# Optimization experiments

Measured on AMD Instinct MI355X. Metric: run time of the kernel, lower is better.

Reference implementation:

```python
import jax, jax.numpy as jnp
import numpy as np

INC, OUTC, NHEADS, KSIZE = 256, 256, 8, 5


def setup_inputs() -> dict:
    key = jax.random.key(0)
    k1, k2 = jax.random.split(key, 2)
    x = jax.random.normal(k1, (4, INC, 64, 64), dtype=jnp.float32)
    w_qkv = jax.random.normal(k2, (3 * OUTC, INC), dtype=jnp.float32) * 0.02
    b_qkv = jnp.zeros((3 * OUTC,), dtype=jnp.float32)
    return {"x": x, "w_qkv": w_qkv, "b_qkv": b_qkv}


def reference(x, w_qkv, b_qkv):
    N, Cin, H, W = x.shape
    hd = OUTC // NHEADS
    ofs = KSIZE // 2
    K2 = KSIZE * KSIZE

    # 1x1 conv == pointwise matmul over channels
    qkv = jnp.einsum('nchw,dc->ndhw', x, w_qkv) + b_qkv[None, :, None, None]
    Q = qkv[:, :OUTC]
    K = qkv[:, OUTC:2 * OUTC]
    V = qkv[:, 2 * OUTC:]

    # Zero-pad K/V; track validity so boundary softmax only spans in-bounds
    # positions (the torch code slices smaller windows at borders -> no pad
    # contribution to softmax).
    Kp = jnp.pad(K, ((0, 0), (0, 0), (ofs, ofs), (ofs, ofs)))
    Vp = jnp.pad(V, ((0, 0), (0, 0), (ofs, ofs), (ofs, ofs)))
    valid = jnp.pad(jnp.ones((H, W), dtype=bool), ((ofs, ofs), (ofs, ofs)))

    # Sliding windows via KSIZE^2 static shifted slices: [N,D,H,W,K2]
    k_win = jnp.stack([Kp[:, :, dy:dy + H, dx:dx + W]
                       for dy in range(KSIZE) for dx in range(KSIZE)], axis=-1)
    v_win = jnp.stack([Vp[:, :, dy:dy + H, dx:dx + W]
                       for dy in range(KSIZE) for dx in range(KSIZE)], axis=-1)
    m_win = jnp.stack([valid[dy:dy + H, dx:dx + W]
                       for dy in range(KSIZE) for dx in range(KSIZE)], axis=-1)  # [H,W,K2]

    qh = Q.reshape(N, NHEADS, hd, H, W)
    kh = k_win.reshape(N, NHEADS, hd, H, W, K2)
    vh = v_win.reshape(N, NHEADS, hd, H, W, K2)

    scores = jnp.einsum('ngdhw,ngdhwk->nghwk', qh, kh)          # [N,G,H,W,K2]
    scores = jnp.where(m_win[None, None], scores, -jnp.inf)
    att = jax.nn.softmax(scores, axis=-1)
    out = jnp.einsum('nghwk,ngdhwk->ngdhw', att, vh)            # [N,G,hd,H,W]
    return out.reshape(N, OUTC, H, W)
```

## Files before the change

### kernel.cpp

```cpp
#include <hip/hip_runtime.h>
#include <hip/hip_bf16.h>
#include <math.h>

#define CIN 256
#define COUT 768
#define OUTC 256
#define HH 64
#define WW 64
#define HW 4096

typedef unsigned int uint32;
typedef unsigned short ushort16;
typedef unsigned long long u64;

using short8 = __attribute__((ext_vector_type(8))) short;
using f32x4  = __attribute__((ext_vector_type(4))) float;
using hf2    = __attribute__((ext_vector_type(2))) _Float16;

__device__ inline uint32 pkbf2(float a, float b) {
    __hip_bfloat162 h = __float22bfloat162_rn(make_float2(a, b));
    union { __hip_bfloat162 h2; uint32 u; } cv; cv.h2 = h;
    return cv.u;
}
__device__ inline uint32 pkhf2(float a, float b) {
    union { _Float16 h[2]; uint32 u; } cv;
    cv.h[0] = (_Float16)a; cv.h[1] = (_Float16)b;
    return cv.u;
}
__device__ inline float dpp_xor1(float x) {
#if __has_builtin(__builtin_amdgcn_update_dpp)
    int i = __builtin_amdgcn_update_dpp(0, __float_as_int(x),
                                        0xB1, 0xF, 0xF, true);
    return __int_as_float(i);
#else
    return __shfl_xor(x, 1, 64);
#endif
}
__device__ inline float dot2acc(hf2 a, hf2 b, float c) {
#if __has_builtin(__builtin_amdgcn_fdot2)
    return __builtin_amdgcn_fdot2(a, b, c, false);
#else
    c = fmaf((float)a[0], (float)b[0], c);
    return fmaf((float)a[1], (float)b[1], c);
#endif
}

#define LDSTR 40

__global__ __launch_bounds__(256) void qkv_gemm_kernel(
    const float* __restrict__ x, const float* __restrict__ wq,
    const float* __restrict__ bq, ushort16* __restrict__ qkv)
{
    __shared__ __align__(16) char smem[32768];
    ushort16* As = (ushort16*)smem;
    ushort16* Bs = (ushort16*)smem + 128 * LDSTR;

    const int n   = blockIdx.z;
    const int d0  = blockIdx.y * 128;
    const int p0  = blockIdx.x * 128;
    const int tid = threadIdx.x;
    const int lane = tid & 63;
    const int wid  = tid >> 6;
    const int wm = wid >> 1;
    const int wn = wid & 1;

    const float* xb = x + (size_t)n * CIN * HW;

    const int arow = tid >> 2;
    const int akk  = (tid & 3) * 8;
    const float* aptr = wq + (size_t)(d0 + arow) * CIN + akk;
    const int bkg = (tid >> 6) * 8;
    const int bpg = (tid & 63) * 2;
    const float* bptr = xb + (size_t)bkg * HW + p0 + bpg;

    ushort16* awr0 = &As[arow * LDSTR + akk];
    ushort16* awr1 = &As[(arow + 64) * LDSTR + akk];
    ushort16* bwr0 = &Bs[bpg * LDSTR + bkg];
    ushort16* bwr1 = &Bs[(bpg + 1) * LDSTR + bkg];

    f32x4 acc[4][4];
    #pragma unroll
    for (int i = 0; i < 4; ++i)
        #pragma unroll
        for (int j = 0; j < 4; ++j) acc[i][j] = (f32x4){0.f, 0.f, 0.f, 0.f};

    const int lrow = lane & 15;
    const int lk   = (lane >> 4) * 8;

    float4 a0[4], a1[4];
    float2 b0[8], b1[8];

#define LOAD_SET(aS, bS, ko) do {                                         \
        aS[0] = *(const float4*)(aptr + (ko));                            \
        aS[1] = *(const float4*)(aptr + (ko) + 4);                        \
        aS[2] = *(const float4*)(aptr + (size_t)64 * CIN + (ko));         \
        aS[3] = *(const float4*)(aptr + (size_t)64 * CIN + (ko) + 4);     \
        _Pragma("unroll")                                                 \
        for (int j = 0; j < 8; ++j)                                       \
            bS[j] = *(const float2*)(bptr + (size_t)((ko) + j) * HW);     \
    } while (0)

#define WRITE_SET(aS, bS) do {                                            \
        uint32 w0 = pkbf2(aS[0].x, aS[0].y), w1 = pkbf2(aS[0].z, aS[0].w);\
        uint32 w2 = pkbf2(aS[1].x, aS[1].y), w3 = pkbf2(aS[1].z, aS[1].w);\
        *(uint4*)awr0 = make_uint4(w0, w1, w2, w3);                       \
        w0 = pkbf2(aS[2].x, aS[2].y); w1 = pkbf2(aS[2].z, aS[2].w);       \
        w2 = pkbf2(aS[3].x, aS[3].y); w3 = pkbf2(aS[3].z, aS[3].w);       \
        *(uint4*)awr1 = make_uint4(w0, w1, w2, w3);                       \
        uint4 c0, c1;                                                     \
        c0.x = pkbf2(bS[0].x, bS[1].x); c0.y = pkbf2(bS[2].x, bS[3].x);   \
        c0.z = pkbf2(bS[4].x, bS[5].x); c0.w = pkbf2(bS[6].x, bS[7].x);   \
        c1.x = pkbf2(bS[0].y, bS[1].y); c1.y = pkbf2(bS[2].y, bS[3].y);   \
        c1.z = pkbf2(bS[4].y, bS[5].y); c1.w = pkbf2(bS[6].y, bS[7].y);   \
        *(uint4*)bwr0 = c0;                                               \
        *(uint4*)bwr1 = c1;                                               \
    } while (0)

#define COMPUTE() do {                                                    \
        short8 af[4], bf[4];                                              \
        _Pragma("unroll")                                                 \
        for (int fm = 0; fm < 4; ++fm)                                    \
            af[fm] = *(const short8*)&As[(wm * 64 + fm * 16 + lrow) * LDSTR + lk]; \
        _Pragma("unroll")                                                 \
        for (int fn = 0; fn < 4; ++fn)                                    \
            bf[fn] = *(const short8*)&Bs[(wn * 64 + fn * 16 + lrow) * LDSTR + lk]; \
        _Pragma("unroll")                                                 \
        for (int fm = 0; fm < 4; ++fm)                                    \
            _Pragma("unroll")                                             \
            for (int fn = 0; fn < 4; ++fn)                                \
                acc[fm][fn] = __builtin_amdgcn_mfma_f32_16x16x32_bf16(    \
                    af[fm], bf[fn], acc[fm][fn], 0, 0, 0);                \
    } while (0)

    LOAD_SET(a0, b0, 0);
    LOAD_SET(a1, b1, 32);

    #pragma unroll 1
    for (int kt = 0; kt < 8; kt += 2) {
        __syncthreads();
        WRITE_SET(a0, b0);
        if (kt + 2 < 8) LOAD_SET(a0, b0, (kt + 2) * 32);
        __syncthreads();
        COMPUTE();

        __syncthreads();
        WRITE_SET(a1, b1);
        if (kt + 3 < 8) LOAD_SET(a1, b1, (kt + 3) * 32);
        __syncthreads();
        COMPUTE();
    }
#undef LOAD_SET
#undef WRITE_SET
#undef COMPUTE

    __syncthreads();

    u64* E = (u64*)smem + (size_t)wid * 1024;

    const int hi4 = lane >> 4;
    #pragma unroll
    for (int fm = 0; fm < 4; ++fm) {
        const int D = d0 + wm * 64 + fm * 16 + hi4 * 4;
        const float4 bias = *(const float4*)(&bq[D]);
        const int cell = fm * 2 + (hi4 >> 1);
        const int half = hi4 & 1;
        #pragma unroll
        for (int fn = 0; fn < 4; ++fn) {
            const int pl = fn * 16 + lrow;
            f32x4 v = acc[fm][fn];
            u64 pk = (u64)pkhf2(v[0] + bias.x, v[1] + bias.y)
                   | ((u64)pkhf2(v[2] + bias.z, v[3] + bias.w) << 32);
            E[pl * 16 + (cell ^ (pl & 7)) * 2 + half] = pk;
        }
    }
    const int pl4 = lane >> 2;
    const int dq  = lane & 3;
    ushort16* qn = qkv + (size_t)n * COUT * HW;
    #pragma unroll
    for (int s = 0; s < 2; ++s) {
        const int D = d0 + wm * 64 + s * 32;
        const int slot = D >> 5;
        ushort16* sb2 = qn + (size_t)slot * (HW * 32);
        #pragma unroll
        for (int g = 0; g < 4; ++g) {
            const int prow = g * 16 + pl4;
            const int c = s * 4 + dq;
            const uint4 val = *(const uint4*)&E[prow * 16 + ((c ^ (prow & 7)) * 2)];
            *(uint4*)(sb2 + (size_t)(p0 + wn * 64 + prow) * 32 + dq * 8) = val;
        }
    }
}

#define TR 4
#define TC 32
#define HR 8
#define HC 36
#define NPIX (HR*HC)

__global__ __launch_bounds__(256) void attn_kernel(
    const ushort16* __restrict__ qkv, float* __restrict__ out)
{
    __shared__ uint4 Ks[NPIX * 4];
    __shared__ uint4 Vs[NPIX * 4];

    const int n    = blockIdx.z;
    const int head = blockIdx.y;
    const int ht = blockIdx.x >> 1;
    const int wt = blockIdx.x & 1;
    const int h0 = ht * TR;
    const int w0 = wt * TC;

    const int tid  = threadIdx.x;
    const int half = tid & 1;
    const int wc   = (tid >> 1) & 31;
    const int tr   = tid >> 6;

    const int h = h0 + tr, w = w0 + wc;
    const int p = h * WW + w;

    const uint4* Kb = (const uint4*)(qkv + ((size_t)(n * 24 + 8 + head)) * HW * 32);
    const uint4* Vb = (const uint4*)(qkv + ((size_t)(n * 24 + 16 + head)) * HW * 32);

    for (int c = tid; c < 2 * NPIX * 4; c += 256) {
        const int b  = (c >= NPIX * 4);
        const int cc = c - b * NPIX * 4;
        const int pix = cc >> 2, i = cc & 3;
        const int hr = pix / HC, cw = pix - hr * HC;
        const int hh = h0 + hr - 2, ww = w0 + cw - 2;
        if (hh >= 0 && hh < HH && ww >= 0 && ww < WW) {
            const int pp = hh * WW + ww;
            const uint4 v = (b ? Vb : Kb)[(size_t)pp * 4 + i];
            const int unit = (pix * 4 + i) ^ (pix & 7);
            (b ? Vs : Ks)[unit] = v;
        }
    }

    hf2 q[8];
    {
        const uint4* Qp = (const uint4*)(qkv + (((size_t)(n * 24 + head)) * HW + p) * 32);
        union { uint4 u; hf2 h[4]; } c0, c1;
        c0.u = Qp[half * 2];
        c1.u = Qp[half * 2 + 1];
        #pragma unroll
        for (int i = 0; i < 4; ++i) { q[i] = c0.h[i]; q[4 + i] = c1.h[i]; }
    }

    __syncthreads();

    float sc[25];
    #pragma unroll
    for (int ky = 0; ky < 5; ++ky) {
        const int hh = h + ky - 2;
        const int hr = tr + ky;
        #pragma unroll
        for (int kx = 0; kx < 5; ++kx) {
            const int ww = w + kx - 2;
            float s;
            if (hh >= 0 && hh < HH && ww >= 0 && ww < WW) {
                const int pix = hr * HC + (wc + kx);
                const int u0 = (pix * 4 + half * 2)     ^ (pix & 7);
                const int u1 = (pix * 4 + half * 2 + 1) ^ (pix & 7);
                union { uint4 u; hf2 h[4]; } a, b;
                a.u = Ks[u0]; b.u = Ks[u1];
                float t = 0.f;
                t = dot2acc(q[0], a.h[0], t);
                t = dot2acc(q[1], a.h[1], t);
                t = dot2acc(q[2], a.h[2], t);
                t = dot2acc(q[3], a.h[3], t);
                t = dot2acc(q[4], b.h[0], t);
                t = dot2acc(q[5], b.h[1], t);
                t = dot2acc(q[6], b.h[2], t);
                t = dot2acc(q[7], b.h[3], t);
                s = t;
            } else {
                s = -1e30f;
            }
            sc[ky * 5 + kx] = s;
        }
    }
    #pragma unroll
    for (int k = 0; k < 25; ++k) {
        float o = dpp_xor1(sc[k]);
        sc[k] = (sc[k] <= -1e29f) ? sc[k] : sc[k] + o;
    }

    float m = sc[0];
    #pragma unroll
    for (int k = 1; k < 25; ++k) m = fmaxf(m, sc[k]);
    float sum = 0.f;
    #pragma unroll
    for (int k = 0; k < 25; ++k) {
        float e = __expf(sc[k] - m);
        sc[k] = e;
        sum += e;
    }
    const float inv = 1.f / sum;

    hf2 acch[8];
    #pragma unroll
    for (int i = 0; i < 8; ++i) acch[i] = (hf2){(_Float16)0.f, (_Float16)0.f};
    #pragma unroll
    for (int ky = 0; ky < 5; ++ky) {
        const int hh = h + ky - 2;
        if (hh < 0 || hh >= HH) continue;
        const int hr = tr + ky;
        #pragma unroll
        for (int kx = 0; kx < 5; ++kx) {
            const int ww = w + kx - 2;
            if (ww < 0 || ww >= WW) continue;
            const _Float16 af = (_Float16)sc[ky * 5 + kx];
            const hf2 ah = (hf2){af, af};
            const int pix = hr * HC + (wc + kx);
            const int u0 = (pix * 4 + half * 2)     ^ (pix & 7);
            const int u1 = (pix * 4 + half * 2 + 1) ^ (pix & 7);
            union { uint4 u; hf2 h[4]; } xv, yv;
            xv.u = Vs[u0]; yv.u = Vs[u1];
            acch[0] += ah * xv.h[0];
            acch[1] += ah * xv.h[1];
            acch[2] += ah * xv.h[2];
            acch[3] += ah * xv.h[3];
            acch[4] += ah * yv.h[0];
            acch[5] += ah * yv.h[1];
            acch[6] += ah * yv.h[2];
            acch[7] += ah * yv.h[3];
        }
    }

    float* Ob = out + ((size_t)(n * 8 + head) * 32 + half * 16) * HW + p;
    #pragma unroll
    for (int i = 0; i < 8; ++i) {
        Ob[(size_t)(2*i)   * HW] = (float)acch[i][0] * inv;
        Ob[(size_t)(2*i+1) * HW] = (float)acch[i][1] * inv;
    }
}

extern "C" void kernel_launch(void* const* d_in, const int* in_sizes, int n_in,
                              void* d_out, int out_size, void* d_ws, size_t ws_size,
                              hipStream_t stream) {
    const float* x  = (const float*)d_in[0];
    const float* wq = (const float*)d_in[1];
    const float* bq = (const float*)d_in[2];
    float* out = (float*)d_out;
    ushort16* qkv = (ushort16*)d_ws;

    dim3 g1(HW / 128, COUT / 128, 4);
    qkv_gemm_kernel<<<g1, 256, 0, stream>>>(x, wq, bq, qkv);

    dim3 g2(32, 8, 4);
    attn_kernel<<<g2, 256, 0, stream>>>(qkv, out);
}
```

Baseline: 41.49 us.

## Split head dim over four lanes, halve attention tile, share one LDS buffer for K then V

The attention kernel now assigns four threads per pixel, each holding 8 of the 32 head channels, and reduces the partial scores with two DPP xor steps. Tiles shrink to 4x16 pixels, so the grid doubles to 2048 blocks. A single shared buffer first holds K, then is refilled with V that was prefetched into registers during the score phase, which cuts LDS per block. Score and AV loops run at raised wave priority. In exchange the halo overhead per pixel grows (20 columns loaded for 16 output) and two extra barriers are added.

```diff
diff --git a/kernel.cpp b/kernel.cpp
--- a/kernel.cpp
+++ b/kernel.cpp
@@ -34,6 +34,15 @@
     return __int_as_float(i);
 #else
     return __shfl_xor(x, 1, 64);
+#endif
+}
+__device__ inline float dpp_xor2(float x) {
+#if __has_builtin(__builtin_amdgcn_update_dpp)
+    int i = __builtin_amdgcn_update_dpp(0, __float_as_int(x),
+                                        0x4E, 0xF, 0xF, true);
+    return __int_as_float(i);
+#else
+    return __shfl_xor(x, 2, 64);
 #endif
 }
 __device__ inline float dot2acc(hf2 a, hf2 b, float c) {
@@ -192,61 +201,72 @@
 }
 
 #define TR 4
-#define TC 32
+#define TC 16
 #define HR 8
-#define HC 36
+#define HC 20
 #define NPIX (HR*HC)
+#define NCELL (NPIX*4)
 
 __global__ __launch_bounds__(256) void attn_kernel(
     const ushort16* __restrict__ qkv, float* __restrict__ out)
 {
-    __shared__ uint4 Ks[NPIX * 4];
-    __shared__ uint4 Vs[NPIX * 4];
+    __shared__ uint4 KVs[NCELL];
 
     const int n    = blockIdx.z;
     const int head = blockIdx.y;
-    const int ht = blockIdx.x >> 1;
-    const int wt = blockIdx.x & 1;
+    const int ht = blockIdx.x >> 2;
+    const int wt = blockIdx.x & 3;
     const int h0 = ht * TR;
     const int w0 = wt * TC;
 
     const int tid  = threadIdx.x;
-    const int half = tid & 1;
-    const int wc   = (tid >> 1) & 31;
-    const int tr   = tid >> 6;
-
+    const int quar = tid & 3;
+    const int pid  = tid >> 2;
+    const int tr = pid >> 4, wc = pid & 15;
     const int h = h0 + tr, w = w0 + wc;
     const int p = h * WW + w;
 
+    const uint4* Qb = (const uint4*)(qkv + ((size_t)(n * 24 + head)) * HW * 32);
     const uint4* Kb = (const uint4*)(qkv + ((size_t)(n * 24 + 8 + head)) * HW * 32);
     const uint4* Vb = (const uint4*)(qkv + ((size_t)(n * 24 + 16 + head)) * HW * 32);
 
-    for (int c = tid; c < 2 * NPIX * 4; c += 256) {
-        const int b  = (c >= NPIX * 4);
-        const int cc = c - b * NPIX * 4;
-        const int pix = cc >> 2, i = cc & 3;
-        const int hr = pix / HC, cw = pix - hr * HC;
-        const int hh = h0 + hr - 2, ww = w0 + cw - 2;
-        if (hh >= 0 && hh < HH && ww >= 0 && ww < WW) {
-            const int pp = hh * WW + ww;
-            const uint4 v = (b ? Vb : Kb)[(size_t)pp * 4 + i];
-            const int unit = (pix * 4 + i) ^ (pix & 7);
-            (b ? Vs : Ks)[unit] = v;
-        }
-    }
-
-    hf2 q[8];
+    #pragma unroll
+    for (int it = 0; it < 3; ++it) {
+        const int c = tid + it * 256;
+        if (c < NCELL) {
+            const int pix = c >> 2, i = c & 3;
+            const int hr = pix / HC, cw = pix - hr * HC;
+            const int hh = h0 + hr - 2, ww = w0 + cw - 2;
+            if (hh >= 0 && hh < HH && ww >= 0 && ww < WW) {
+                const int pp = hh * WW + ww;
+                KVs[(pix * 4 + i) ^ (pix & 7)] = Kb[(size_t)pp * 4 + i];
+            }
+        }
+    }
+    uint4 vreg[3];
+    #pragma unroll
+    for (int it = 0; it < 3; ++it) {
+        const int c = tid + it * 256;
+        if (c < NCELL) {
+            const int pix = c >> 2, i = c & 3;
+            const int hr = pix / HC, cw = pix - hr * HC;
+            const int hh = h0 + hr - 2, ww = w0 + cw - 2;
+            if (hh >= 0 && hh < HH && ww >= 0 && ww < WW)
+                vreg[it] = Vb[(size_t)(hh * WW + ww) * 4 + i];
+        }
+    }
+
+    hf2 q[4];
     {
-        const uint4* Qp = (const uint4*)(qkv + (((size_t)(n * 24 + head)) * HW + p) * 32);
-        union { uint4 u; hf2 h[4]; } c0, c1;
-        c0.u = Qp[half * 2];
-        c1.u = Qp[half * 2 + 1];
-        #pragma unroll
-        for (int i = 0; i < 4; ++i) { q[i] = c0.h[i]; q[4 + i] = c1.h[i]; }
+        union { uint4 u; hf2 h[4]; } c;
+        c.u = Qb[(size_t)p * 4 + quar];
+        #pragma unroll
+        for (int i = 0; i < 4; ++i) q[i] = c.h[i];
     }
 
     __syncthreads();
 
+    __builtin_amdgcn_s_setprio(1);
     float sc[25];
     #pragma unroll
     for (int ky = 0; ky < 5; ++ky) {
@@ -255,33 +275,36 @@
         #pragma unroll
         for (int kx = 0; kx < 5; ++kx) {
             const int ww = w + kx - 2;
-            float s;
-            if (hh >= 0 && hh < HH && ww >= 0 && ww < WW) {
+            const bool valid = (hh >= 0 && hh < HH && ww >= 0 && ww < WW);
+            float t = 0.f;
+            if (valid) {
                 const int pix = hr * HC + (wc + kx);
-                const int u0 = (pix * 4 + half * 2)     ^ (pix & 7);
-                const int u1 = (pix * 4 + half * 2 + 1) ^ (pix & 7);
-                union { uint4 u; hf2 h[4]; } a, b;
-                a.u = Ks[u0]; b.u = Ks[u1];
-                float t = 0.f;
-                t = dot2acc(q[0], a.h[0], t);
-                t = dot2acc(q[1], a.h[1], t);
-                t = dot2acc(q[2], a.h[2], t);
-                t = dot2acc(q[3], a.h[3], t);
-                t = dot2acc(q[4], b.h[0], t);
-                t = dot2acc(q[5], b.h[1], t);
-                t = dot2acc(q[6], b.h[2], t);
-                t = dot2acc(q[7], b.h[3], t);
-                s = t;
-            } else {
-                s = -1e30f;
+                union { uint4 u; hf2 hh2[4]; } a;
+                a.u = KVs[(pix * 4 + quar) ^ (pix & 7)];
+                t = dot2acc(q[0], a.hh2[0], t);
+                t = dot2acc(q[1], a.hh2[1], t);
+                t = dot2acc(q[2], a.hh2[2], t);
+                t = dot2acc(q[3], a.hh2[3], t);
             }
-            sc[ky * 5 + kx] = s;
-        }
-    }
-    #pragma unroll
-    for (int k = 0; k < 25; ++k) {
-        float o = dpp_xor1(sc[k]);
-        sc[k] = (sc[k] <= -1e29f) ? sc[k] : sc[k] + o;
+            t += dpp_xor1(t);
+            t += dpp_xor2(t);
+            sc[ky * 5 + kx] = valid ? t : -1e30f;
+        }
+    }
+    __builtin_amdgcn_s_setprio(0);
+
+    __syncthreads();
+
+    #pragma unroll
+    for (int it = 0; it < 3; ++it) {
+        const int c = tid + it * 256;
+        if (c < NCELL) {
+            const int pix = c >> 2, i = c & 3;
+            const int hr = pix / HC, cw = pix - hr * HC;
+            const int hh = h0 + hr - 2, ww = w0 + cw - 2;
+            if (hh >= 0 && hh < HH && ww >= 0 && ww < WW)
+                KVs[(pix * 4 + i) ^ (pix & 7)] = vreg[it];
+        }
     }
 
     float m = sc[0];
@@ -296,9 +319,12 @@
     }
     const float inv = 1.f / sum;
 
-    hf2 acch[8];
-    #pragma unroll
-    for (int i = 0; i < 8; ++i) acch[i] = (hf2){(_Float16)0.f, (_Float16)0.f};
+    __syncthreads();
+
+    __builtin_amdgcn_s_setprio(1);
+    hf2 acch[4];
+    #pragma unroll
+    for (int i = 0; i < 4; ++i) acch[i] = (hf2){(_Float16)0.f, (_Float16)0.f};
     #pragma unroll
     for (int ky = 0; ky < 5; ++ky) {
         const int hh = h + ky - 2;
@@ -311,24 +337,19 @@
             const _Float16 af = (_Float16)sc[ky * 5 + kx];
             const hf2 ah = (hf2){af, af};
             const int pix = hr * HC + (wc + kx);
-            const int u0 = (pix * 4 + half * 2)     ^ (pix & 7);
-            const int u1 = (pix * 4 + half * 2 + 1) ^ (pix & 7);
-            union { uint4 u; hf2 h[4]; } xv, yv;
-            xv.u = Vs[u0]; yv.u = Vs[u1];
-            acch[0] += ah * xv.h[0];
-            acch[1] += ah * xv.h[1];
-            acch[2] += ah * xv.h[2];
-            acch[3] += ah * xv.h[3];
-            acch[4] += ah * yv.h[0];
-            acch[5] += ah * yv.h[1];
-            acch[6] += ah * yv.h[2];
-            acch[7] += ah * yv.h[3];
-        }
-    }
-
-    float* Ob = out + ((size_t)(n * 8 + head) * 32 + half * 16) * HW + p;
-    #pragma unroll
-    for (int i = 0; i < 8; ++i) {
+            union { uint4 u; hf2 hh2[4]; } v;
+            v.u = KVs[(pix * 4 + quar) ^ (pix & 7)];
+            acch[0] += ah * v.hh2[0];
+            acch[1] += ah * v.hh2[1];
+            acch[2] += ah * v.hh2[2];
+            acch[3] += ah * v.hh2[3];
+        }
+    }
+    __builtin_amdgcn_s_setprio(0);
+
+    float* Ob = out + ((size_t)(n * 8 + head) * 32 + quar * 8) * HW + p;
+    #pragma unroll
+    for (int i = 0; i < 4; ++i) {
         Ob[(size_t)(2*i)   * HW] = (float)acch[i][0] * inv;
         Ob[(size_t)(2*i+1) * HW] = (float)acch[i][1] * inv;
     }
@@ -346,6 +367,6 @@
     dim3 g1(HW / 128, COUT / 128, 4);
     qkv_gemm_kernel<<<g1, 256, 0, stream>>>(x, wq, bq, qkv);
 
-    dim3 g2(32, 8, 4);
+    dim3 g2(64, 8, 4);
     attn_kernel<<<g2, 256, 0, stream>>>(qkv, out);
 }
```

After: 49.38 us. +19.0%, slower.

## Process two adjacent pixels per thread and reuse K/V window cells in registers

Applied to the files above, without the earlier changes.

The attention kernel now tiles full 64-wide rows (halo 68), so the grid halves, and each thread handles two horizontally adjacent pixels. Per window row it loads 6 K/V cells from shared memory into registers and reuses them for both pixels' 5 taps, cutting LDS reads. Out-of-bounds halo cells are zero-filled and masked after the score reduction, the swizzle changes to pair granularity, and outputs are written as float2. It leaves a dead first V-accumulation loop that is later overwritten, which wastes work unless the compiler removes it. Register pressure also rises.

```diff
diff --git a/kernel.cpp b/kernel.cpp
--- a/kernel.cpp
+++ b/kernel.cpp
@@ -192,145 +192,204 @@
 }
 
 #define TR 4
-#define TC 32
+#define HC 68
 #define HR 8
-#define HC 36
 #define NPIX (HR*HC)
+#define NCELL (NPIX*4)
 
 __global__ __launch_bounds__(256) void attn_kernel(
     const ushort16* __restrict__ qkv, float* __restrict__ out)
 {
-    __shared__ uint4 Ks[NPIX * 4];
-    __shared__ uint4 Vs[NPIX * 4];
+    __shared__ uint4 Ks[NCELL];
+    __shared__ uint4 Vs[NCELL];
 
     const int n    = blockIdx.z;
     const int head = blockIdx.y;
-    const int ht = blockIdx.x >> 1;
-    const int wt = blockIdx.x & 1;
-    const int h0 = ht * TR;
-    const int w0 = wt * TC;
+    const int h0   = blockIdx.x * TR;
 
     const int tid  = threadIdx.x;
     const int half = tid & 1;
-    const int wc   = (tid >> 1) & 31;
+    const int g    = (tid >> 1) & 31;
     const int tr   = tid >> 6;
 
-    const int h = h0 + tr, w = w0 + wc;
-    const int p = h * WW + w;
-
+    const int h  = h0 + tr;
+    const int w0q = 2 * g;
+
+    const uint4* Qb = (const uint4*)(qkv + ((size_t)(n * 24 + head)) * HW * 32);
     const uint4* Kb = (const uint4*)(qkv + ((size_t)(n * 24 + 8 + head)) * HW * 32);
     const uint4* Vb = (const uint4*)(qkv + ((size_t)(n * 24 + 16 + head)) * HW * 32);
 
-    for (int c = tid; c < 2 * NPIX * 4; c += 256) {
-        const int b  = (c >= NPIX * 4);
-        const int cc = c - b * NPIX * 4;
-        const int pix = cc >> 2, i = cc & 3;
+    const uint4 zero4 = make_uint4(0u, 0u, 0u, 0u);
+    for (int c = tid; c < 2 * NCELL; c += 256) {
+        const int b  = (c >= NCELL);
+        const int cc = c - b * NCELL;
+        const int pix = cc >> 2, u = cc & 3;
         const int hr = pix / HC, cw = pix - hr * HC;
-        const int hh = h0 + hr - 2, ww = w0 + cw - 2;
-        if (hh >= 0 && hh < HH && ww >= 0 && ww < WW) {
-            const int pp = hh * WW + ww;
-            const uint4 v = (b ? Vb : Kb)[(size_t)pp * 4 + i];
-            const int unit = (pix * 4 + i) ^ (pix & 7);
-            (b ? Vs : Ks)[unit] = v;
-        }
-    }
-
-    hf2 q[8];
+        const int hh = h0 + hr - 2, ww = cw - 2;
+        const int unit = (pix * 4 + u) ^ ((pix >> 1) & 7);
+        uint4 v = zero4;
+        if (hh >= 0 && hh < HH && ww >= 0 && ww < WW)
+            v = (b ? Vb : Kb)[(size_t)(hh * WW + ww) * 4 + u];
+        (b ? Vs : Ks)[unit] = v;
+    }
+
+    hf2 q0[8], q1[8];
     {
-        const uint4* Qp = (const uint4*)(qkv + (((size_t)(n * 24 + head)) * HW + p) * 32);
-        union { uint4 u; hf2 h[4]; } c0, c1;
-        c0.u = Qp[half * 2];
-        c1.u = Qp[half * 2 + 1];
-        #pragma unroll
-        for (int i = 0; i < 4; ++i) { q[i] = c0.h[i]; q[4 + i] = c1.h[i]; }
+        const size_t pbase = (size_t)(h * WW + w0q) * 4 + half * 2;
+        union { uint4 u; hf2 h2[4]; } c;
+        c.u = Qb[pbase + 0];
+        #pragma unroll
+        for (int i = 0; i < 4; ++i) q0[i] = c.h2[i];
+        c.u = Qb[pbase + 1];
+        #pragma unroll
+        for (int i = 0; i < 4; ++i) q0[4 + i] = c.h2[i];
+        c.u = Qb[pbase + 4];
+        #pragma unroll
+        for (int i = 0; i < 4; ++i) q1[i] = c.h2[i];
+        c.u = Qb[pbase + 5];
+        #pragma unroll
+        for (int i = 0; i < 4; ++i) q1[4 + i] = c.h2[i];
     }
 
     __syncthreads();
 
-    float sc[25];
+    float sc0[25], sc1[25];
+    #pragma unroll
+    for (int ky = 0; ky < 5; ++ky) {
+        const int hr = tr + ky;
+        union { uint4 u; hf2 h2[4]; } cell[12];
+        #pragma unroll
+        for (int c = 0; c < 6; ++c) {
+            const int pix = hr * HC + w0q + c;
+            const int swz = (pix >> 1) & 7;
+            cell[c * 2 + 0].u = Ks[(pix * 4 + half * 2 + 0) ^ swz];
+            cell[c * 2 + 1].u = Ks[(pix * 4 + half * 2 + 1) ^ swz];
+        }
+        #pragma unroll
+        for (int kx = 0; kx < 5; ++kx) {
+            float t0 = 0.f, t1 = 0.f;
+            #pragma unroll
+            for (int i = 0; i < 4; ++i) {
+                t0 = dot2acc(q0[i],     cell[kx * 2 + 0].h2[i], t0);
+                t0 = dot2acc(q0[4 + i], cell[kx * 2 + 1].h2[i], t0);
+                t1 = dot2acc(q1[i],     cell[(kx + 1) * 2 + 0].h2[i], t1);
+                t1 = dot2acc(q1[4 + i], cell[(kx + 1) * 2 + 1].h2[i], t1);
+            }
+            sc0[ky * 5 + kx] = t0;
+            sc1[ky * 5 + kx] = t1;
+        }
+    }
+
     #pragma unroll
     for (int ky = 0; ky < 5; ++ky) {
         const int hh = h + ky - 2;
+        const bool hok = (hh >= 0 && hh < HH);
+        #pragma unroll
+        for (int kx = 0; kx < 5; ++kx) {
+            const int k = ky * 5 + kx;
+            const int ww0 = w0q + kx - 2;
+            float t0 = sc0[k] + dpp_xor1(sc0[k]);
+            float t1 = sc1[k] + dpp_xor1(sc1[k]);
+            sc0[k] = (hok && ww0 >= 0 && ww0 < WW) ? t0 : -1e30f;
+            sc1[k] = (hok && ww0 + 1 >= 0 && ww0 + 1 < WW) ? t1 : -1e30f;
+        }
+    }
+
+    float m0 = sc0[0], m1 = sc1[0];
+    #pragma unroll
+    for (int k = 1; k < 25; ++k) { m0 = fmaxf(m0, sc0[k]); m1 = fmaxf(m1, sc1[k]); }
+    float sum0 = 0.f, sum1 = 0.f;
+    #pragma unroll
+    for (int k = 0; k < 25; ++k) {
+        float e0 = __expf(sc0[k] - m0); sc0[k] = e0; sum0 += e0;
+        float e1 = __expf(sc1[k] - m1); sc1[k] = e1; sum1 += e1;
+    }
+    const float inv0 = 1.f / sum0;
+    const float inv1 = 1.f / sum1;
+
+    hf2 acc0[4], acc1[4];
+    #pragma unroll
+    for (int i = 0; i < 4; ++i) {
+        acc0[i] = (hf2){(_Float16)0.f, (_Float16)0.f};
+        acc1[i] = (hf2){(_Float16)0.f, (_Float16)0.f};
+    }
+    #pragma unroll
+    for (int ky = 0; ky < 5; ++ky) {
         const int hr = tr + ky;
+        union { uint4 u; hf2 h2[4]; } cell[12];
+        #pragma unroll
+        for (int c = 0; c < 6; ++c) {
+            const int pix = hr * HC + w0q + c;
+            const int swz = (pix >> 1) & 7;
+            cell[c * 2 + 0].u = Vs[(pix * 4 + half * 2 + 0) ^ swz];
+            cell[c * 2 + 1].u = Vs[(pix * 4 + half * 2 + 1) ^ swz];
+        }
         #pragma unroll
         for (int kx = 0; kx < 5; ++kx) {
-            const int ww = w + kx - 2;
-            float s;
-            if (hh >= 0 && hh < HH && ww >= 0 && ww < WW) {
-                const int pix = hr * HC + (wc + kx);
-                const int u0 = (pix * 4 + half * 2)     ^ (pix & 7);
-                const int u1 = (pix * 4 + half * 2 + 1) ^ (pix & 7);
-                union { uint4 u; hf2 h[4]; } a, b;
-                a.u = Ks[u0]; b.u = Ks[u1];
-                float t = 0.f;
-                t = dot2acc(q[0], a.h[0], t);
-                t = dot2acc(q[1], a.h[1], t);
-                t = dot2acc(q[2], a.h[2], t);
-                t = dot2acc(q[3], a.h[3], t);
-                t = dot2acc(q[4], b.h[0], t);
-                t = dot2acc(q[5], b.h[1], t);
-                t = dot2acc(q[6], b.h[2], t);
-                t = dot2acc(q[7], b.h[3], t);
-                s = t;
-            } else {
-                s = -1e30f;
+            const int k = ky * 5 + kx;
+            const _Float16 a0 = (_Float16)sc0[k];
+            const _Float16 a1 = (_Float16)sc1[k];
+            const hf2 ah0 = (hf2){a0, a0};
+            const hf2 ah1 = (hf2){a1, a1};
+            #pragma unroll
+            for (int i = 0; i < 4; ++i) {
+                acc0[i] += ah0 * cell[kx * 2 + (i >> 1)].h2[(i & 1) * 2 + 0];
+                acc0[i] += ah0 * (hf2){(_Float16)0.f, (_Float16)0.f};
             }
-            sc[ky * 5 + kx] = s;
-        }
-    }
-    #pragma unroll
-    for (int k = 0; k < 25; ++k) {
-        float o = dpp_xor1(sc[k]);
-        sc[k] = (sc[k] <= -1e29f) ? sc[k] : sc[k] + o;
-    }
-
-    float m = sc[0];
-    #pragma unroll
-    for (int k = 1; k < 25; ++k) m = fmaxf(m, sc[k]);
-    float sum = 0.f;
-    #pragma unroll
-    for (int k = 0; k < 25; ++k) {
-        float e = __expf(sc[k] - m);
-        sc[k] = e;
-        sum += e;
-    }
-    const float inv = 1.f / sum;
-
-    hf2 acch[8];
-    #pragma unroll
-    for (int i = 0; i < 8; ++i) acch[i] = (hf2){(_Float16)0.f, (_Float16)0.f};
+        }
+    }
+
+    #pragma unroll
+    for (int i = 0; i < 4; ++i) {
+        acc0[i] = (hf2){(_Float16)0.f, (_Float16)0.f};
+        acc1[i] = (hf2){(_Float16)0.f, (_Float16)0.f};
+    }
+    hf2 acc0b[4], acc1b[4];
+    #pragma unroll
+    for (int i = 0; i < 4; ++i) {
+        acc0b[i] = (hf2){(_Float16)0.f, (_Float16)0.f};
+        acc1b[i] = (hf2){(_Float16)0.f, (_Float16)0.f};
+    }
     #pragma unroll
     for (int ky = 0; ky < 5; ++ky) {
-        const int hh = h + ky - 2;
-        if (hh < 0 || hh >= HH) continue;
         const int hr = tr + ky;
+        union { uint4 u; hf2 h2[4]; } cell[12];
+        #pragma unroll
+        for (int c = 0; c < 6; ++c) {
+            const int pix = hr * HC + w0q + c;
+            const int swz = (pix >> 1) & 7;
+            cell[c * 2 + 0].u = Vs[(pix * 4 + half * 2 + 0) ^ swz];
+            cell[c * 2 + 1].u = Vs[(pix * 4 + half * 2 + 1) ^ swz];
+        }
         #pragma unroll
         for (int kx = 0; kx < 5; ++kx) {
-            const int ww = w + kx - 2;
-            if (ww < 0 || ww >= WW) continue;
-            const _Float16 af = (_Float16)sc[ky * 5 + kx];
-            const hf2 ah = (hf2){af, af};
-            const int pix = hr * HC + (wc + kx);
-            const int u0 = (pix * 4 + half * 2)     ^ (pix & 7);
-            const int u1 = (pix * 4 + half * 2 + 1) ^ (pix & 7);
-            union { uint4 u; hf2 h[4]; } xv, yv;
-            xv.u = Vs[u0]; yv.u = Vs[u1];
-            acch[0] += ah * xv.h[0];
-            acch[1] += ah * xv.h[1];
-            acch[2] += ah * xv.h[2];
-            acch[3] += ah * xv.h[3];
-            acch[4] += ah * yv.h[0];
-            acch[5] += ah * yv.h[1];
-            acch[6] += ah * yv.h[2];
-            acch[7] += ah * yv.h[3];
-        }
-    }
-
-    float* Ob = out + ((size_t)(n * 8 + head) * 32 + half * 16) * HW + p;
-    #pragma unroll
-    for (int i = 0; i < 8; ++i) {
-        Ob[(size_t)(2*i)   * HW] = (float)acch[i][0] * inv;
-        Ob[(size_t)(2*i+1) * HW] = (float)acch[i][1] * inv;
+            const int k = ky * 5 + kx;
+            const _Float16 a0 = (_Float16)sc0[k];
+            const _Float16 a1 = (_Float16)sc1[k];
+            const hf2 ah0 = (hf2){a0, a0};
+            const hf2 ah1 = (hf2){a1, a1};
+            #pragma unroll
+            for (int i = 0; i < 4; ++i) {
+                acc0[i]  += ah0 * cell[kx * 2 + 0].h2[i];
+                acc0b[i] += ah0 * cell[kx * 2 + 1].h2[i];
+                acc1[i]  += ah1 * cell[(kx + 1) * 2 + 0].h2[i];
+                acc1b[i] += ah1 * cell[(kx + 1) * 2 + 1].h2[i];
+            }
+        }
+    }
+
+    float* Ob = out + ((size_t)(n * 8 + head) * 32 + half * 16) * HW
+                    + h * WW + w0q;
+    #pragma unroll
+    for (int i = 0; i < 4; ++i) {
+        *(float2*)&Ob[(size_t)(2 * i) * HW] =
+            make_float2((float)acc0[i][0] * inv0, (float)acc1[i][0] * inv1);
+        *(float2*)&Ob[(size_t)(2 * i + 1) * HW] =
+            make_float2((float)acc0[i][1] * inv0, (float)acc1[i][1] * inv1);
+        *(float2*)&Ob[(size_t)(8 + 2 * i) * HW] =
+            make_float2((float)acc0b[i][0] * inv0, (float)acc1b[i][0] * inv1);
+        *(float2*)&Ob[(size_t)(8 + 2 * i + 1) * HW] =
+            make_float2((float)acc0b[i][1] * inv0, (float)acc1b[i][1] * inv1);
     }
 }
 
@@ -346,6 +405,6 @@
     dim3 g1(HW / 128, COUT / 128, 4);
     qkv_gemm_kernel<<<g1, 256, 0, stream>>>(x, wq, bq, qkv);
 
-    dim3 g2(32, 8, 4);
+    dim3 g2(16, 8, 4);
     attn_kernel<<<g2, 256, 0, stream>>>(qkv, out);
 }
```

Measured after the change: 41.83 us. Within noise of the previous version (+0.8%).

## Rewrite neighborhood attention to use MFMA on 4x4 query tiles per wave

Applied to the files above, without the earlier changes.

The attention kernel now assigns each wave a 4x4 query tile and its 8x8 key/value halo. QK scores and the PV product are computed with 16x16x32 f16 MFMA instructions instead of per-thread dot2 and packed-half FMAs. The 5x5 window is masked inside the dense 16x64 score tile, and V is transposed into LDS for the B operand. This cuts scalar ALU work, but the halo is recomputed per wave, so each wave redundantly loads K/V and does more raw FLOPs. It also adds shuffles to rearrange the probabilities.

```diff
diff --git a/kernel.cpp b/kernel.cpp
--- a/kernel.cpp
+++ b/kernel.cpp
@@ -15,7 +15,7 @@
 
 using short8 = __attribute__((ext_vector_type(8))) short;
 using f32x4  = __attribute__((ext_vector_type(4))) float;
-using hf2    = __attribute__((ext_vector_type(2))) _Float16;
+using hf8    = __attribute__((ext_vector_type(8))) _Float16;
 
 __device__ inline uint32 pkbf2(float a, float b) {
     __hip_bfloat162 h = __float22bfloat162_rn(make_float2(a, b));
@@ -26,23 +26,6 @@
     union { _Float16 h[2]; uint32 u; } cv;
     cv.h[0] = (_Float16)a; cv.h[1] = (_Float16)b;
     return cv.u;
-}
-__device__ inline float dpp_xor1(float x) {
-#if __has_builtin(__builtin_amdgcn_update_dpp)
-    int i = __builtin_amdgcn_update_dpp(0, __float_as_int(x),
-                                        0xB1, 0xF, 0xF, true);
-    return __int_as_float(i);
-#else
-    return __shfl_xor(x, 1, 64);
-#endif
-}
-__device__ inline float dot2acc(hf2 a, hf2 b, float c) {
-#if __has_builtin(__builtin_amdgcn_fdot2)
-    return __builtin_amdgcn_fdot2(a, b, c, false);
-#else
-    c = fmaf((float)a[0], (float)b[0], c);
-    return fmaf((float)a[1], (float)b[1], c);
-#endif
 }
 
 #define LDSTR 40
@@ -191,146 +174,142 @@
     }
 }
 
-#define TR 4
-#define TC 32
-#define HR 8
-#define HC 36
-#define NPIX (HR*HC)
-
 __global__ __launch_bounds__(256) void attn_kernel(
     const ushort16* __restrict__ qkv, float* __restrict__ out)
 {
-    __shared__ uint4 Ks[NPIX * 4];
-    __shared__ uint4 Vs[NPIX * 4];
+    __shared__ uint4 sh[4 * 544];
 
     const int n    = blockIdx.z;
     const int head = blockIdx.y;
-    const int ht = blockIdx.x >> 1;
-    const int wt = blockIdx.x & 1;
-    const int h0 = ht * TR;
-    const int w0 = wt * TC;
+    const int qby  = blockIdx.x >> 2;
+    const int qbxg = blockIdx.x & 3;
 
     const int tid  = threadIdx.x;
-    const int half = tid & 1;
-    const int wc   = (tid >> 1) & 31;
-    const int tr   = tid >> 6;
-
-    const int h = h0 + tr, w = w0 + wc;
-    const int p = h * WW + w;
-
+    const int wid  = tid >> 6;
+    const int lane = tid & 63;
+
+    const int h0  = qby * 4;
+    const int w0q = (qbxg * 4 + wid) * 4;
+
+    uint4* Ksw = sh + wid * 544;
+    uint4* Vtw = Ksw + 256;
+    _Float16* Vt16 = (_Float16*)Vtw;
+
+    const uint4* Qb = (const uint4*)(qkv + ((size_t)(n * 24 + head)) * HW * 32);
     const uint4* Kb = (const uint4*)(qkv + ((size_t)(n * 24 + 8 + head)) * HW * 32);
     const uint4* Vb = (const uint4*)(qkv + ((size_t)(n * 24 + 16 + head)) * HW * 32);
 
-    for (int c = tid; c < 2 * NPIX * 4; c += 256) {
-        const int b  = (c >= NPIX * 4);
-        const int cc = c - b * NPIX * 4;
-        const int pix = cc >> 2, i = cc & 3;
-        const int hr = pix / HC, cw = pix - hr * HC;
-        const int hh = h0 + hr - 2, ww = w0 + cw - 2;
-        if (hh >= 0 && hh < HH && ww >= 0 && ww < WW) {
-            const int pp = hh * WW + ww;
-            const uint4 v = (b ? Vb : Kb)[(size_t)pp * 4 + i];
-            const int unit = (pix * 4 + i) ^ (pix & 7);
-            (b ? Vs : Ks)[unit] = v;
-        }
-    }
-
-    hf2 q[8];
     {
-        const uint4* Qp = (const uint4*)(qkv + (((size_t)(n * 24 + head)) * HW + p) * 32);
-        union { uint4 u; hf2 h[4]; } c0, c1;
-        c0.u = Qp[half * 2];
-        c1.u = Qp[half * 2 + 1];
-        #pragma unroll
-        for (int i = 0; i < 4; ++i) { q[i] = c0.h[i]; q[4 + i] = c1.h[i]; }
-    }
-
-    __syncthreads();
-
-    float sc[25];
-    #pragma unroll
-    for (int ky = 0; ky < 5; ++ky) {
-        const int hh = h + ky - 2;
-        const int hr = tr + ky;
-        #pragma unroll
-        for (int kx = 0; kx < 5; ++kx) {
-            const int ww = w + kx - 2;
-            float s;
-            if (hh >= 0 && hh < HH && ww >= 0 && ww < WW) {
-                const int pix = hr * HC + (wc + kx);
-                const int u0 = (pix * 4 + half * 2)     ^ (pix & 7);
-                const int u1 = (pix * 4 + half * 2 + 1) ^ (pix & 7);
-                union { uint4 u; hf2 h[4]; } a, b;
-                a.u = Ks[u0]; b.u = Ks[u1];
-                float t = 0.f;
-                t = dot2acc(q[0], a.h[0], t);
-                t = dot2acc(q[1], a.h[1], t);
-                t = dot2acc(q[2], a.h[2], t);
-                t = dot2acc(q[3], a.h[3], t);
-                t = dot2acc(q[4], b.h[0], t);
-                t = dot2acc(q[5], b.h[1], t);
-                t = dot2acc(q[6], b.h[2], t);
-                t = dot2acc(q[7], b.h[3], t);
-                s = t;
-            } else {
-                s = -1e30f;
-            }
-            sc[ky * 5 + kx] = s;
-        }
-    }
-    #pragma unroll
-    for (int k = 0; k < 25; ++k) {
-        float o = dpp_xor1(sc[k]);
-        sc[k] = (sc[k] <= -1e29f) ? sc[k] : sc[k] + o;
-    }
-
-    float m = sc[0];
-    #pragma unroll
-    for (int k = 1; k < 25; ++k) m = fmaxf(m, sc[k]);
+        const int wy = lane >> 3, wx = lane & 7;
+        const int gh = h0 + wy - 2, gw = w0q + wx - 2;
+        const bool inb = (gh >= 0) && (gh < HH) && (gw >= 0) && (gw < WW);
+        const size_t gp = inb ? (size_t)(gh * WW + gw) * 4 : 0;
+        const uint4 z4 = make_uint4(0u, 0u, 0u, 0u);
+        uint4 kv[4];
+        union { uint4 v[4]; _Float16 h[32]; } V;
+        #pragma unroll
+        for (int u = 0; u < 4; ++u) {
+            kv[u]  = inb ? Kb[gp + u] : z4;
+            V.v[u] = inb ? Vb[gp + u] : z4;
+        }
+        #pragma unroll
+        for (int u = 0; u < 4; ++u)
+            Ksw[lane * 4 + (u ^ ((lane >> 1) & 3))] = kv[u];
+        #pragma unroll
+        for (int d = 0; d < 32; ++d)
+            Vt16[d * 72 + lane] = V.h[d];
+    }
+
+    const int q  = lane & 15;
+    const int hi = lane >> 4;
+    const int qy = q >> 2, qx = q & 3;
+
+    union { uint4 u; hf8 h; } Bq;
+    Bq.u = Qb[(size_t)((h0 + qy) * WW + (w0q + qx)) * 4 + hi];
+
+    f32x4 S[4];
+    #pragma unroll
+    for (int g = 0; g < 4; ++g) {
+        const int px = g * 16 + q;
+        union { uint4 u; hf8 h; } Ka;
+        Ka.u = Ksw[px * 4 + (hi ^ ((px >> 1) & 3))];
+        S[g] = __builtin_amdgcn_mfma_f32_16x16x32_f16(
+            Ka.h, Bq.h, (f32x4){0.f, 0.f, 0.f, 0.f}, 0, 0, 0);
+    }
+
+    float e[4][4];
+    float mx = -1e30f;
+    #pragma unroll
+    for (int g = 0; g < 4; ++g)
+        #pragma unroll
+        for (int r = 0; r < 4; ++r) {
+            const int t  = 4 * hi + r;
+            const int wy = 2 * g + (t >> 3);
+            const int wx = t & 7;
+            const bool valid =
+                ((unsigned)(wy - qy) <= 4u) && ((unsigned)(wx - qx) <= 4u) &&
+                ((unsigned)(h0 + wy - 2) < (unsigned)HH) &&
+                ((unsigned)(w0q + wx - 2) < (unsigned)WW);
+            const float s = valid ? S[g][r] : -1e30f;
+            e[g][r] = s;
+            mx = fmaxf(mx, s);
+        }
+    mx = fmaxf(mx, __shfl_xor(mx, 16, 64));
+    mx = fmaxf(mx, __shfl_xor(mx, 32, 64));
     float sum = 0.f;
     #pragma unroll
-    for (int k = 0; k < 25; ++k) {
-        float e = __expf(sc[k] - m);
-        sc[k] = e;
-        sum += e;
-    }
+    for (int g = 0; g < 4; ++g)
+        #pragma unroll
+        for (int r = 0; r < 4; ++r) {
+            const float t = __expf(e[g][r] - mx);
+            e[g][r] = t;
+            sum += t;
+        }
+    sum += __shfl_xor(sum, 16, 64);
+    sum += __shfl_xor(sum, 32, 64);
     const float inv = 1.f / sum;
 
-    hf2 acch[8];
-    #pragma unroll
-    for (int i = 0; i < 8; ++i) acch[i] = (hf2){(_Float16)0.f, (_Float16)0.f};
-    #pragma unroll
-    for (int ky = 0; ky < 5; ++ky) {
-        const int hh = h + ky - 2;
-        if (hh < 0 || hh >= HH) continue;
-        const int hr = tr + ky;
-        #pragma unroll
-        for (int kx = 0; kx < 5; ++kx) {
-            const int ww = w + kx - 2;
-            if (ww < 0 || ww >= WW) continue;
-            const _Float16 af = (_Float16)sc[ky * 5 + kx];
-            const hf2 ah = (hf2){af, af};
-            const int pix = hr * HC + (wc + kx);
-            const int u0 = (pix * 4 + half * 2)     ^ (pix & 7);
-            const int u1 = (pix * 4 + half * 2 + 1) ^ (pix & 7);
-            union { uint4 u; hf2 h[4]; } xv, yv;
-            xv.u = Vs[u0]; yv.u = Vs[u1];
-            acch[0] += ah * xv.h[0];
-            acch[1] += ah * xv.h[1];
-            acch[2] += ah * xv.h[2];
-            acch[3] += ah * xv.h[3];
-            acch[4] += ah * yv.h[0];
-            acch[5] += ah * yv.h[1];
-            acch[6] += ah * yv.h[2];
-            acch[7] += ah * yv.h[3];
-        }
-    }
-
-    float* Ob = out + ((size_t)(n * 8 + head) * 32 + half * 16) * HW + p;
-    #pragma unroll
-    for (int i = 0; i < 8; ++i) {
-        Ob[(size_t)(2*i)   * HW] = (float)acch[i][0] * inv;
-        Ob[(size_t)(2*i+1) * HW] = (float)acch[i][1] * inv;
+    uint32 pk[4][2];
+    #pragma unroll
+    for (int g = 0; g < 4; ++g) {
+        pk[g][0] = pkhf2(e[g][0], e[g][1]);
+        pk[g][1] = pkhf2(e[g][2], e[g][3]);
+    }
+
+    f32x4 O[2] = {(f32x4){0.f, 0.f, 0.f, 0.f}, (f32x4){0.f, 0.f, 0.f, 0.f}};
+    #pragma unroll
+    for (int cc = 0; cc < 2; ++cc) {
+        union { uint32 w[4]; hf8 h; } A;
+        #pragma unroll
+        for (int w = 0; w < 4; ++w) {
+            const int b  = w >> 1, pi = w & 1;
+            const int sl = q + 16 * ((2 * hi + b) & 3);
+            const uint32 lo  = (uint32)__shfl((int)pk[2 * cc][pi],     sl, 64);
+            const uint32 hi2 = (uint32)__shfl((int)pk[2 * cc + 1][pi], sl, 64);
+            A.w[w] = (hi >= 2) ? hi2 : lo;
+        }
+        #pragma unroll
+        for (int nt = 0; nt < 2; ++nt) {
+            union { uint4 u; hf8 h; } Bv;
+            Bv.u = *(const uint4*)(Vt16 + (nt * 16 + q) * 72 + cc * 32 + hi * 8);
+            O[nt] = __builtin_amdgcn_mfma_f32_16x16x32_f16(
+                A.h, Bv.h, O[nt], 0, 0, 0);
+        }
+    }
+
+    float invr[4];
+    #pragma unroll
+    for (int r = 0; r < 4; ++r)
+        invr[r] = __shfl(inv, hi * 4 + r, 64);
+
+    float* Ob = out + (size_t)((n * 8 + head) * 32) * HW;
+    #pragma unroll
+    for (int r = 0; r < 4; ++r) {
+        const int qq = hi * 4 + r;
+        const int pp = (h0 + (qq >> 2)) * WW + (w0q + (qq & 3));
+        #pragma unroll
+        for (int nt = 0; nt < 2; ++nt)
+            Ob[(size_t)(nt * 16 + q) * HW + pp] = O[nt][r] * invr[r];
     }
 }
 
@@ -346,6 +325,6 @@
     dim3 g1(HW / 128, COUT / 128, 4);
     qkv_gemm_kernel<<<g1, 256, 0, stream>>>(x, wq, bq, qkv);
 
-    dim3 g2(32, 8, 4);
+    dim3 g2(64, 8, 4);
     attn_kernel<<<g2, 256, 0, stream>>>(qkv, out);
 }
```

Result: slower. 63.90 us (+54.0%).
